# Optimization experiments

Hardware: AMD Instinct MI355X
Metric: run time of the kernel (lower is better)

## Reference

```python
import jax, jax.numpy as jnp
import numpy as np

B, T, D = 64, 2048, 512
C, K = 4, 128            # num_codebooks, codebook_size
d = D // C               # per-codebook dim = 128
COMMITMENT_COST = 0.25


def setup_inputs() -> dict:
    key = jax.random.key(0)
    k1, k2 = jax.random.split(key)
    inputs = jax.random.normal(k1, (B, T, D), dtype=jnp.float32)
    # torch init: randn(K, d) * 4, one table per codebook -> stacked [C, K, d]
    embeddings = jax.random.normal(k2, (C, K, d), dtype=jnp.float32) * 4.0
    return {"inputs": inputs, "embeddings": embeddings}


def reference(inputs, embeddings):
    input_shape = inputs.shape
    # flatten tokens and split feature dim into C codebook slots: [N, C, d]
    x = inputs.reshape(-1, C, d)
    # squared L2 distances per codebook: [N, C, K]
    x2 = jnp.sum(x * x, axis=-1, keepdims=True)            # [N, C, 1]
    e2 = jnp.sum(embeddings * embeddings, axis=-1)          # [C, K]
    dots = jnp.einsum('ncd,ckd->nck', x, embeddings)        # [N, C, K]
    distances = x2 + e2[None, :, :] - 2.0 * dots
    idx = jnp.argmin(distances, axis=-1)                    # [N, C] int
    # direct gather instead of one-hot matmul (same math)
    quantized = embeddings[jnp.arange(C)[None, :], idx]     # [N, C, d]
    quantized = quantized.reshape(input_shape)
    # squared-l2 VQ loss per position
    e_latent = jnp.sum((jax.lax.stop_gradient(quantized) - inputs) ** 2, axis=-1)
    q_latent = jnp.sum((quantized - jax.lax.stop_gradient(inputs)) ** 2, axis=-1)
    quantization_loss = q_latent + COMMITMENT_COST * e_latent
    # straight-through estimator
    quantized_sg = inputs + jax.lax.stop_gradient(quantized - inputs)
    # combined product code: fold base-K digits, matches torch loop order
    powers = K ** jnp.arange(C - 1, -1, -1, dtype=jnp.int32)  # [C]
    encoding_indices = jnp.sum(idx.astype(jnp.int32) * powers, axis=-1, keepdims=True)  # [N, 1]
    return quantized_sg, encoding_indices, quantization_loss
```

## Files before the change

### kernel.cpp

```cpp
#include <hip/hip_runtime.h>


#define NTOK 131072
#define DF   512
#define CS   4
#define DS   128
#define KC   128
#define PITCH 136
#define TAU  0.5f

typedef _Float16 half8 __attribute__((ext_vector_type(8)));
typedef float   f32x4 __attribute__((ext_vector_type(4)));

__global__ __launch_bounds__(256, 4)
void pvq_main(const float* __restrict__ inp, const float* __restrict__ emb,
              float* __restrict__ outq, int* __restrict__ idx_ws,
              float* __restrict__ dist_ws) {
  __shared__ _Float16 elds[KC * PITCH];
  __shared__ float    e2s[KC];

  const int c    = blockIdx.y;
  const int t    = threadIdx.x;
  const int lane = t & 63;
  const int wid  = t >> 6;
  const int nf   = lane & 15;
  const int quad = lane >> 4;

  const float* ebase = emb + (size_t)c * KC * DS;

  {
    const float4* eg = (const float4*)ebase;
    #pragma unroll
    for (int it = 0; it < 16; ++it) {
      int i = it * 256 + t;
      float4 v = eg[i];
      int code = i >> 5;
      int dpos = (i & 31) << 2;
      _Float16* p = &elds[code * PITCH + dpos];
      p[0] = (_Float16)v.x; p[1] = (_Float16)v.y;
      p[2] = (_Float16)v.z; p[3] = (_Float16)v.w;
    }
    if (t < KC) {
      const float4* er = (const float4*)(ebase + (size_t)t * DS);
      float s = 0.f;
      #pragma unroll 8
      for (int i = 0; i < 32; ++i) {
        float4 v = er[i];
        s = fmaf(v.x, v.x, s); s = fmaf(v.y, v.y, s);
        s = fmaf(v.z, v.z, s); s = fmaf(v.w, v.w, s);
      }
      e2s[t] = 0.5f * s;
    }
  }
  __syncthreads();

  float e2r[8];
  #pragma unroll
  for (int nt = 0; nt < 8; ++nt) e2r[nt] = e2s[nt * 16 + nf];

  const int rowblk = blockIdx.x * 256 + wid * 64;
  for (int tile = 0; tile < 4; ++tile) {
    const int n0 = rowblk + tile * 16;
    const float* xrow = inp + (size_t)(n0 + nf) * DF + c * DS;

    half8 afrag[4];
    float x2 = 0.f;
    #pragma unroll
    for (int kc4 = 0; kc4 < 4; ++kc4) {
      const float4* xp = (const float4*)(xrow + kc4 * 32 + quad * 8);
      float4 v0 = xp[0], v1 = xp[1];
      x2 = fmaf(v0.x, v0.x, x2); x2 = fmaf(v0.y, v0.y, x2);
      x2 = fmaf(v0.z, v0.z, x2); x2 = fmaf(v0.w, v0.w, x2);
      x2 = fmaf(v1.x, v1.x, x2); x2 = fmaf(v1.y, v1.y, x2);
      x2 = fmaf(v1.z, v1.z, x2); x2 = fmaf(v1.w, v1.w, x2);
      afrag[kc4][0] = (_Float16)v0.x; afrag[kc4][1] = (_Float16)v0.y;
      afrag[kc4][2] = (_Float16)v0.z; afrag[kc4][3] = (_Float16)v0.w;
      afrag[kc4][4] = (_Float16)v1.x; afrag[kc4][5] = (_Float16)v1.y;
      afrag[kc4][6] = (_Float16)v1.z; afrag[kc4][7] = (_Float16)v1.w;
    }
    x2 += __shfl_xor(x2, 16);
    x2 += __shfl_xor(x2, 32);

    f32x4 acc[8];
    #pragma unroll
    for (int nt = 0; nt < 8; ++nt) acc[nt] = (f32x4){0.f, 0.f, 0.f, 0.f};
    #pragma unroll
    for (int nt = 0; nt < 8; ++nt) {
      #pragma unroll
      for (int kc4 = 0; kc4 < 4; ++kc4) {
        half8 b = *(const half8*)&elds[(nt * 16 + nf) * PITCH + kc4 * 32 + quad * 8];
        acc[nt] = __builtin_amdgcn_mfma_f32_16x16x32_f16(afrag[kc4], b, acc[nt], 0, 0, 0);
      }
    }

    float s1[4], s2[4]; int k1[4], k2[4];
    #pragma unroll
    for (int r = 0; r < 4; ++r) { s1[r] = 1e30f; s2[r] = 1e30f; k1[r] = 0; k2[r] = 0; }
    #pragma unroll
    for (int nt = 0; nt < 8; ++nt) {
      int kidx = nt * 16 + nf;
      #pragma unroll
      for (int r = 0; r < 4; ++r) {
        float s = e2r[nt] - acc[nt][r];
        if (s < s1[r])      { s2[r] = s1[r]; k2[r] = k1[r]; s1[r] = s; k1[r] = kidx; }
        else if (s < s2[r]) { s2[r] = s;     k2[r] = kidx; }
      }
    }
    #pragma unroll
    for (int off = 1; off < 16; off <<= 1) {
      #pragma unroll
      for (int r = 0; r < 4; ++r) {
        float o1 = __shfl_xor(s1[r], off); int ok1 = __shfl_xor(k1[r], off);
        float o2 = __shfl_xor(s2[r], off); int ok2 = __shfl_xor(k2[r], off);
        bool takeo = (o1 < s1[r]) || (o1 == s1[r] && ok1 < k1[r]);
        float w1 = takeo ? o1 : s1[r]; int wk1 = takeo ? ok1 : k1[r];
        float l1 = takeo ? s1[r] : o1; int lk1 = takeo ? k1[r] : ok1;
        float n2 = l1; int nk2 = lk1;
        if (s2[r] < n2) { n2 = s2[r]; nk2 = k2[r]; }
        if (o2 < n2)    { n2 = o2;    nk2 = ok2;  }
        s1[r] = w1; k1[r] = wk1; s2[r] = n2; k2[r] = nk2;
      }
    }

    #pragma unroll 1
    for (int r = 0; r < 16; ++r) {
      const int srcl = (r >> 2) * 16;
      float s1r = __shfl(s1[r & 3], srcl);
      int   kb  = __shfl(k1[r & 3], srcl);
      float s2r = __shfl(s2[r & 3], srcl);
      int   kb2 = __shfl(k2[r & 3], srcl);
      float x2r = __shfl(x2, r);
      const int n = n0 + r;
      float p;
      if (s2r - s1r < TAU) {
        const float2* xp = (const float2*)(inp + (size_t)n * DF + c * DS);
        const float2* eA = (const float2*)(ebase + (size_t)kb  * DS);
        const float2* eB = (const float2*)(ebase + (size_t)kb2 * DS);
        float2 xv = xp[lane], a = eA[lane], b = eB[lane];
        double pA = (double)(xv.x - a.x) * (xv.x - a.x) + (double)(xv.y - a.y) * (xv.y - a.y);
        double pB = (double)(xv.x - b.x) * (xv.x - b.x) + (double)(xv.y - b.y) * (xv.y - b.y);
        #pragma unroll
        for (int off = 1; off < 64; off <<= 1) {
          pA += __shfl_xor(pA, off);
          pB += __shfl_xor(pB, off);
        }
        if (pB < pA || (pB == pA && kb2 < kb)) { kb = kb2; p = (float)pB; }
        else                                   { p = (float)pA; }
      } else {
        p = x2r + 2.f * s1r;
      }
      const float2* ef = (const float2*)(ebase + (size_t)kb * DS);
      float2 q = ef[lane];
      *(float2*)(outq + (size_t)n * DF + c * DS + 2 * lane) = q;
      if (lane == r) { idx_ws[n * CS + c] = kb; dist_ws[n * CS + c] = p; }
    }
  }
}

__global__ void pvq_tail(const int* __restrict__ idx_ws,
                         const float* __restrict__ dist_ws,
                         float* __restrict__ out_enc,
                         float* __restrict__ out_loss) {
  int n = blockIdx.x * blockDim.x + threadIdx.x;
  if (n >= NTOK) return;
  int4   k  = *(const int4*)&idx_ws[(size_t)n * 4];
  float4 dv = *(const float4*)&dist_ws[(size_t)n * 4];
  int enc = ((k.x * KC + k.y) * KC + k.z) * KC + k.w;
  out_enc[n]  = (float)enc;
  out_loss[n] = 1.25f * (((dv.x + dv.y) + dv.z) + dv.w);
}

extern "C" void kernel_launch(void* const* d_in, const int* in_sizes, int n_in,
                              void* d_out, int out_size, void* d_ws, size_t ws_size,
                              hipStream_t stream) {
  const float* inp = (const float*)d_in[0];
  const float* emb = (const float*)d_in[1];

  float* outq     = (float*)d_out;
  float* out_enc  = outq + (size_t)NTOK * DF;
  float* out_loss = out_enc + NTOK;

  int*   idx_ws  = (int*)d_ws;
  float* dist_ws = (float*)d_ws + (size_t)NTOK * CS;

  dim3 grid(NTOK / 256, CS);
  pvq_main<<<grid, 256, 0, stream>>>(inp, emb, outq, idx_ws, dist_ws);
  pvq_tail<<<(NTOK + 255) / 256, 256, 0, stream>>>(idx_ws, dist_ws, out_enc, out_loss);
}
```

Measured before the change: 690.9 us.

## Process epilogue rows in parallel per 16-lane group and use 512-thread blocks

The serial 16-row epilogue loop, which broadcast each row's winner and ran a 64-lane reduction plus a narrow float2 store, becomes per-quad processing. Each 16-lane group handles its own 4 rows with float4 loads and stores and a 16-lane double reduction. Blocks grow to 512 threads with each wave covering 32 rows, and the MFMA accumulation is fused with the top-2 selection so only one accumulator stays live. The aims are to remove serialized shuffle-heavy epilogue work, cut register pressure and raise occupancy, at the cost of more per-lane loads for the rescoring path.

```diff
diff --git a/kernel.cpp b/kernel.cpp
--- a/kernel.cpp
+++ b/kernel.cpp
@@ -12,7 +12,19 @@
 typedef _Float16 half8 __attribute__((ext_vector_type(8)));
 typedef float   f32x4 __attribute__((ext_vector_type(4)));
 
-__global__ __launch_bounds__(256, 4)
+__device__ __forceinline__ double sq8(float4 x0, float4 x1, float4 a0, float4 a1) {
+  double s = (double)(x0.x - a0.x) * (x0.x - a0.x);
+  s += (double)(x0.y - a0.y) * (x0.y - a0.y);
+  s += (double)(x0.z - a0.z) * (x0.z - a0.z);
+  s += (double)(x0.w - a0.w) * (x0.w - a0.w);
+  s += (double)(x1.x - a1.x) * (x1.x - a1.x);
+  s += (double)(x1.y - a1.y) * (x1.y - a1.y);
+  s += (double)(x1.z - a1.z) * (x1.z - a1.z);
+  s += (double)(x1.w - a1.w) * (x1.w - a1.w);
+  return s;
+}
+
+__global__ __launch_bounds__(512, 8)
 void pvq_main(const float* __restrict__ inp, const float* __restrict__ emb,
               float* __restrict__ outq, int* __restrict__ idx_ws,
               float* __restrict__ dist_ws) {
@@ -31,8 +43,8 @@
   {
     const float4* eg = (const float4*)ebase;
     #pragma unroll
-    for (int it = 0; it < 16; ++it) {
-      int i = it * 256 + t;
+    for (int it = 0; it < 8; ++it) {
+      int i = it * 512 + t;
       float4 v = eg[i];
       int code = i >> 5;
       int dpos = (i & 31) << 2;
@@ -54,12 +66,9 @@
   }
   __syncthreads();
 
-  float e2r[8];
-  #pragma unroll
-  for (int nt = 0; nt < 8; ++nt) e2r[nt] = e2s[nt * 16 + nf];
-
-  const int rowblk = blockIdx.x * 256 + wid * 64;
-  for (int tile = 0; tile < 4; ++tile) {
+  const int rowblk = blockIdx.x * 256 + wid * 32;
+  #pragma unroll 1
+  for (int tile = 0; tile < 2; ++tile) {
     const int n0 = rowblk + tile * 16;
     const float* xrow = inp + (size_t)(n0 + nf) * DF + c * DS;
 
@@ -81,31 +90,27 @@
     x2 += __shfl_xor(x2, 16);
     x2 += __shfl_xor(x2, 32);
 
-    f32x4 acc[8];
-    #pragma unroll
-    for (int nt = 0; nt < 8; ++nt) acc[nt] = (f32x4){0.f, 0.f, 0.f, 0.f};
+    float s1[4], s2[4]; int k1[4], k2[4];
+    #pragma unroll
+    for (int r = 0; r < 4; ++r) { s1[r] = 1e30f; s2[r] = 1e30f; k1[r] = 0; k2[r] = 0; }
     #pragma unroll
     for (int nt = 0; nt < 8; ++nt) {
+      f32x4 acc = (f32x4){0.f, 0.f, 0.f, 0.f};
       #pragma unroll
       for (int kc4 = 0; kc4 < 4; ++kc4) {
         half8 b = *(const half8*)&elds[(nt * 16 + nf) * PITCH + kc4 * 32 + quad * 8];
-        acc[nt] = __builtin_amdgcn_mfma_f32_16x16x32_f16(afrag[kc4], b, acc[nt], 0, 0, 0);
-      }
-    }
-
-    float s1[4], s2[4]; int k1[4], k2[4];
-    #pragma unroll
-    for (int r = 0; r < 4; ++r) { s1[r] = 1e30f; s2[r] = 1e30f; k1[r] = 0; k2[r] = 0; }
-    #pragma unroll
-    for (int nt = 0; nt < 8; ++nt) {
-      int kidx = nt * 16 + nf;
+        acc = __builtin_amdgcn_mfma_f32_16x16x32_f16(afrag[kc4], b, acc, 0, 0, 0);
+      }
+      const float e2v = e2s[nt * 16 + nf];
+      const int kidx = nt * 16 + nf;
       #pragma unroll
       for (int r = 0; r < 4; ++r) {
-        float s = e2r[nt] - acc[nt][r];
+        float s = e2v - acc[r];
         if (s < s1[r])      { s2[r] = s1[r]; k2[r] = k1[r]; s1[r] = s; k1[r] = kidx; }
         else if (s < s2[r]) { s2[r] = s;     k2[r] = kidx; }
       }
     }
+
     #pragma unroll
     for (int off = 1; off < 16; off <<= 1) {
       #pragma unroll
@@ -122,37 +127,52 @@
       }
     }
 
-    #pragma unroll 1
-    for (int r = 0; r < 16; ++r) {
-      const int srcl = (r >> 2) * 16;
-      float s1r = __shfl(s1[r & 3], srcl);
-      int   kb  = __shfl(k1[r & 3], srcl);
-      float s2r = __shfl(s2[r & 3], srcl);
-      int   kb2 = __shfl(k2[r & 3], srcl);
-      float x2r = __shfl(x2, r);
-      const int n = n0 + r;
-      float p;
-      if (s2r - s1r < TAU) {
-        const float2* xp = (const float2*)(inp + (size_t)n * DF + c * DS);
-        const float2* eA = (const float2*)(ebase + (size_t)kb  * DS);
-        const float2* eB = (const float2*)(ebase + (size_t)kb2 * DS);
-        float2 xv = xp[lane], a = eA[lane], b = eB[lane];
-        double pA = (double)(xv.x - a.x) * (xv.x - a.x) + (double)(xv.y - a.y) * (xv.y - a.y);
-        double pB = (double)(xv.x - b.x) * (xv.x - b.x) + (double)(xv.y - b.y) * (xv.y - b.y);
+    int kbv[4]; float pv[4];
+    #pragma unroll
+    for (int r = 0; r < 4; ++r) {
+      const int row = quad * 4 + r;
+      const float x2r = __shfl(x2, row);
+      if (s2[r] - s1[r] < TAU) {
+        int kb = k1[r], kb2 = k2[r];
+        const float4* xp = (const float4*)(inp + (size_t)(n0 + row) * DF + c * DS);
+        const float4* eA = (const float4*)(ebase + (size_t)kb  * DS);
+        const float4* eB = (const float4*)(ebase + (size_t)kb2 * DS);
+        float4 x0 = xp[2 * nf], x1v = xp[2 * nf + 1];
+        float4 a0 = eA[2 * nf], a1 = eA[2 * nf + 1];
+        float4 b0 = eB[2 * nf], b1 = eB[2 * nf + 1];
+        double pA = sq8(x0, x1v, a0, a1);
+        double pB = sq8(x0, x1v, b0, b1);
         #pragma unroll
-        for (int off = 1; off < 64; off <<= 1) {
+        for (int off = 1; off < 16; off <<= 1) {
           pA += __shfl_xor(pA, off);
           pB += __shfl_xor(pB, off);
         }
-        if (pB < pA || (pB == pA && kb2 < kb)) { kb = kb2; p = (float)pB; }
-        else                                   { p = (float)pA; }
+        if (pB < pA || (pB == pA && kb2 < kb)) { kbv[r] = kb2; pv[r] = (float)pB; }
+        else                                   { kbv[r] = kb;  pv[r] = (float)pA; }
       } else {
-        p = x2r + 2.f * s1r;
-      }
-      const float2* ef = (const float2*)(ebase + (size_t)kb * DS);
-      float2 q = ef[lane];
-      *(float2*)(outq + (size_t)n * DF + c * DS + 2 * lane) = q;
-      if (lane == r) { idx_ws[n * CS + c] = kb; dist_ws[n * CS + c] = p; }
+        kbv[r] = k1[r];
+        pv[r]  = x2r + 2.f * s1[r];
+      }
+    }
+
+    #pragma unroll
+    for (int rb = 0; rb < 4; rb += 2) {
+      const float4* e0 = (const float4*)(ebase + (size_t)kbv[rb]     * DS);
+      const float4* e1 = (const float4*)(ebase + (size_t)kbv[rb + 1] * DS);
+      float4 q0a = e0[2 * nf], q0b = e0[2 * nf + 1];
+      float4 q1a = e1[2 * nf], q1b = e1[2 * nf + 1];
+      float4* o0 = (float4*)(outq + (size_t)(n0 + quad * 4 + rb)     * DF + c * DS);
+      float4* o1 = (float4*)(outq + (size_t)(n0 + quad * 4 + rb + 1) * DF + c * DS);
+      o0[2 * nf] = q0a; o0[2 * nf + 1] = q0b;
+      o1[2 * nf] = q1a; o1[2 * nf + 1] = q1b;
+    }
+    if (nf == 0) {
+      #pragma unroll
+      for (int r = 0; r < 4; ++r) {
+        const int n = n0 + quad * 4 + r;
+        idx_ws[n * CS + c]  = kbv[r];
+        dist_ws[n * CS + c] = pv[r];
+      }
     }
   }
 }
@@ -184,6 +204,6 @@
   float* dist_ws = (float*)d_ws + (size_t)NTOK * CS;
 
   dim3 grid(NTOK / 256, CS);
-  pvq_main<<<grid, 256, 0, stream>>>(inp, emb, outq, idx_ws, dist_ws);
+  pvq_main<<<grid, 512, 0, stream>>>(inp, emb, outq, idx_ws, dist_ws);
   pvq_tail<<<(NTOK + 255) / 256, 256, 0, stream>>>(idx_ws, dist_ws, out_enc, out_loss);
 }
```

Measured after the change: 959.2 us. 38.8% more time.
